# Kernel optimization log

Hardware: AMD Instinct MI355X
Metric: run time of the kernel (lower is better)

## Reference

```python
import jax, jax.numpy as jnp
import numpy as np

B, T, C = 8, 2048, 512
H = 16
HS = C // H  # 32, must equal HEAD_SIZE
TM_DIM = 32   # TIME_MIX_EXTRA_DIM
TD_DIM = 64   # TIME_DECAY_EXTRA_DIM
LAYER_ID, N_LAYER = 5, 12


def setup_inputs() -> dict:
    key = jax.random.key(0)
    ks = jax.random.split(key, 16)
    r01 = LAYER_ID / (N_LAYER - 1)
    r1a0 = 1.0 - LAYER_ID / N_LAYER
    ddd = (jnp.arange(C, dtype=jnp.float32) / C)
    n = jnp.arange(C, dtype=jnp.float32)
    decay_speed = -6.0 + 5.0 * (n / (C - 1)) ** (0.7 + 1.3 * r01)
    zigzag = ((n + 1) % 3 - 1) * 0.1
    faaaa = (r01 * (1 - n / (C - 1)) + zigzag).reshape(H, HS)
    s = 1.0 / np.sqrt(C)
    return {
        "x": jax.random.normal(ks[0], (B, T, C), dtype=jnp.float32),
        "time_maa_x": 1.0 - ddd ** r1a0,
        "time_maa_w": 1.0 - ddd ** r1a0,
        "time_maa_k": 1.0 - ddd ** r1a0,
        "time_maa_v": 1.0 - (ddd ** r1a0 + 0.3 * r01),
        "time_maa_r": 1.0 - ddd ** (0.5 * r1a0),
        "time_maa_g": 1.0 - ddd ** (0.5 * r1a0),
        "time_maa_w1": jax.random.uniform(ks[1], (C, TM_DIM * 5), minval=-1e-4, maxval=1e-4),
        "time_maa_w2": jax.random.uniform(ks[2], (5, TM_DIM, C), minval=-1e-4, maxval=1e-4),
        "time_decay": decay_speed,
        "time_decay_w1": jax.random.uniform(ks[3], (C, TD_DIM), minval=-1e-4, maxval=1e-4),
        "time_decay_w2": jax.random.uniform(ks[4], (TD_DIM, C), minval=-1e-4, maxval=1e-4),
        "time_faaaa": faaaa,
        "Wr": jax.random.normal(ks[5], (C, C)) * s,
        "Wk": jax.random.normal(ks[6], (C, C)) * s,
        "Wv": jax.random.normal(ks[7], (C, C)) * s,
        "Wg": jax.random.normal(ks[8], (C, C)) * s,
        "Wo": jax.random.normal(ks[9], (C, C)) * s,
        "ln_w": jnp.ones((C,), dtype=jnp.float32),
        "ln_b": jnp.zeros((C,), dtype=jnp.float32),
    }


def _wkv6(r, k, v, w, u):
    # r,k,v,w: (B,T,C); u: (H,HS). Linear recurrence per (batch, head).
    rs = r.reshape(B, T, H, HS).transpose(1, 0, 2, 3)
    ks_ = k.reshape(B, T, H, HS).transpose(1, 0, 2, 3)
    vs = v.reshape(B, T, H, HS).transpose(1, 0, 2, 3)
    # decay = exp(-exp(w)) per channel (the kernel passes ew = -exp(w))
    ds = jnp.exp(-jnp.exp(w.astype(jnp.float32))).reshape(B, T, H, HS).transpose(1, 0, 2, 3)
    ub = u[None, :, :, None]  # (1,H,HS_key,1)

    def step(S, inp):  # S: (B,H,HS_key,HS_val)
        r_t, k_t, v_t, d_t = inp
        kv = jnp.einsum("bhj,bhi->bhji", k_t, v_t)
        y = jnp.einsum("bhj,bhji->bhi", r_t, S + ub * kv)
        S = d_t[..., None] * S + kv
        return S, y

    S0 = jnp.zeros((B, H, HS, HS), dtype=jnp.float32)
    _, ys = jax.lax.scan(step, S0, (rs, ks_, vs, ds))
    return ys.transpose(1, 0, 2, 3).reshape(B, T, C)


def reference(x, time_maa_x, time_maa_w, time_maa_k, time_maa_v, time_maa_r,
              time_maa_g, time_maa_w1, time_maa_w2, time_decay, time_decay_w1,
              time_decay_w2, time_faaaa, Wr, Wk, Wv, Wg, Wo, ln_w, ln_b):
    # time shift: x_{t-1}, zeros at t=0  (ZeroPad2d((0,0,1,-1)))
    xshift = jnp.concatenate([jnp.zeros_like(x[:, :1]), x[:, :-1]], axis=1)
    xx = xshift - x
    xxx = x + xx * time_maa_x
    mix = jnp.tanh(jnp.einsum("btc,cd->btd", xxx, time_maa_w1)).reshape(B, T, 5, TM_DIM)
    mix = jnp.einsum("btfd,fdc->fbtc", mix, time_maa_w2)  # (5,B,T,C)
    mw, mk, mv, mr, mg = mix[0], mix[1], mix[2], mix[3], mix[4]
    xw = x + xx * (time_maa_w + mw)
    xk = x + xx * (time_maa_k + mk)
    xv = x + xx * (time_maa_v + mv)
    xr = x + xx * (time_maa_r + mr)
    xg = x + xx * (time_maa_g + mg)
    r = xr @ Wr.T
    k = xk @ Wk.T
    v = xv @ Wv.T
    g = jax.nn.silu(xg @ Wg.T)
    w = time_decay + jnp.tanh(xw @ time_decay_w1) @ time_decay_w2
    y = _wkv6(r, k, v, w, time_faaaa)
    # GroupNorm with H groups over channel dim, eps=1e-5
    yg = y.reshape(B, T, H, HS)
    mu = yg.mean(-1, keepdims=True)
    var = yg.var(-1, keepdims=True)
    yn = ((yg - mu) * jax.lax.rsqrt(var + 1e-5)).reshape(B, T, C)
    yn = yn * ln_w + ln_b
    return (yn * g) @ Wo.T
```

## Files before the change

kernel.cpp:

```cpp
#include <hip/hip_runtime.h>
#include <hip/hip_bf16.h>

#define B_ 8
#define T_ 2048
#define C_ 512
#define H_ 16
#define HS_ 32
#define BT_ (B_*T_)
#define CL_ 64
#define NC_ (T_/CL_)
#define STF_ 1056
#define WSZ_ 262144

typedef __hip_bfloat16 bf16;
typedef __attribute__((ext_vector_type(8))) short short8;
typedef __attribute__((ext_vector_type(4))) short short4v;
typedef __attribute__((ext_vector_type(4))) float f32x4;

__device__ __forceinline__ float b2f(bf16 v) { return __bfloat162float(v); }
__device__ __forceinline__ bf16 f2b(float v) { return __float2bfloat16(v); }
__device__ __forceinline__ float s2f(short s) {
  unsigned u = ((unsigned)(unsigned short)s) << 16;
  return __builtin_bit_cast(float, u);
}
__device__ __forceinline__ short f2s(float f) {
  bf16 b = f2b(f);
  return __builtin_bit_cast(short, b);
}

__device__ __forceinline__ void gl2lds(const void* g, void* l) {
  __builtin_amdgcn_global_load_lds(
      (const __attribute__((address_space(1))) void*)g,
      (__attribute__((address_space(3))) void*)l, 16, 0, 0);
}

__global__ __launch_bounds__(256) void prep_combo_kernel(
    const float* __restrict__ x, const float* __restrict__ tmx,
    const float* __restrict__ Wr, const float* __restrict__ Wk,
    const float* __restrict__ Wv, const float* __restrict__ Wg,
    const float* __restrict__ Wo, const float* __restrict__ w1,
    const float* __restrict__ wd1, const float* __restrict__ w2,
    bf16* __restrict__ xxx, bf16* __restrict__ Wrb, bf16* __restrict__ Wkb,
    bf16* __restrict__ Wvb, bf16* __restrict__ Wgb, bf16* __restrict__ Wob,
    bf16* __restrict__ w1p, bf16* __restrict__ wd1p, bf16* __restrict__ w2p) {
  int idx = blockIdx.x * 256 + threadIdx.x;
  if (idx < BT_ * C_) {
    int c = idx & (C_ - 1);
    int t = (idx >> 9) & (T_ - 1);
    float xc = x[idx];
    float xp = (t == 0) ? 0.f : x[idx - C_];
    xxx[idx] = f2b(xc + (xp - xc) * tmx[c]);
    return;
  }
  idx -= BT_ * C_;
  if (idx < 5 * WSZ_) {
    int w = idx >> 18;
    int i = idx & (WSZ_ - 1);
    const float* src = (w == 0) ? Wr : (w == 1) ? Wk : (w == 2) ? Wv
                     : (w == 3) ? Wg : Wo;
    bf16* dst = (w == 0) ? Wrb : (w == 1) ? Wkb : (w == 2) ? Wvb
              : (w == 3) ? Wgb : Wob;
    float s = src[i];
    bf16 hi = f2b(s);
    dst[i] = hi;
    dst[WSZ_ + i] = f2b(s - b2f(hi));
    return;
  }
  idx -= 5 * WSZ_;
  if (idx < 192 * 512) {
    int n = idx >> 9, k = idx & (C_ - 1);
    w1p[idx] = f2b(n < 160 ? w1[k * 160 + n] : 0.f);
    return;
  }
  idx -= 192 * 512;
  if (idx < 64 * 512) {
    int n = idx >> 9, k = idx & (C_ - 1);
    wd1p[idx] = f2b(wd1[k * 64 + n]);
    return;
  }
  idx -= 64 * 512;
  {
    int c = idx / 192, n = idx - c * 192;
    w2p[idx] = f2b(n < 160 ? w2[(size_t)n * C_ + c] : 0.f);
  }
}
#define PREP_N_ ((BT_*C_ + 5*WSZ_ + 192*512 + 64*512 + 512*192) / 256)

template<int BN, int MODE, int SPLIT>
__global__ __launch_bounds__(256) void mfma_gemm_kernel(
    const bf16* __restrict__ A, const bf16* __restrict__ Bw,
    void* __restrict__ O, int N) {
  constexpr int BM = 128, BK = 32;
  constexpr int AE = BM * BK / 8;
  constexpr int BE = BN * BK / 8;
  __shared__ short8 Asm[AE];
  __shared__ short8 Bsm[BE];
  __shared__ short8 Lsm[SPLIT ? BE : 1];
  const int tid = threadIdx.x;
  const int lane = tid & 63;
  const int wave = tid >> 6;
  const int m0 = blockIdx.x * BM;
  const int n0 = blockIdx.y * BN;
  const int wm = (BN == 128) ? (wave >> 1) * 64 : wave * 32;
  const int wn = (BN == 128) ? (wave & 1) * 64 : 0;
  constexpr int MT = (BN == 128) ? 4 : 2;
  constexpr int NT = 4;
  f32x4 acc[MT][NT] = {};
  const int e0 = tid, e1 = tid + 256;
  const int r0 = ((e0 >> 6) << 4) | (e0 & 15), q0 = (e0 >> 4) & 3;
  const int r1 = ((e1 >> 6) << 4) | (e1 & 15), q1 = (e1 >> 4) & 3;
  const unsigned short* Au = (const unsigned short*)A;
  const unsigned short* Bu = (const unsigned short*)Bw;
  const unsigned short* Lu = Bu + (SPLIT ? WSZ_ : 0);
  for (int k0 = 0; k0 < C_; k0 += BK) {
    __syncthreads();
    gl2lds(&Au[(size_t)(m0 + r0) * C_ + k0 + q0 * 8], &Asm[e0]);
    gl2lds(&Au[(size_t)(m0 + r1) * C_ + k0 + q1 * 8], &Asm[e1]);
    gl2lds(&Bu[(size_t)(n0 + r0) * C_ + k0 + q0 * 8], &Bsm[e0]);
    if constexpr (BN == 128)
      gl2lds(&Bu[(size_t)(n0 + r1) * C_ + k0 + q1 * 8], &Bsm[e1]);
    if constexpr (SPLIT) {
      gl2lds(&Lu[(size_t)(n0 + r0) * C_ + k0 + q0 * 8], &Lsm[e0]);
      if constexpr (BN == 128)
        gl2lds(&Lu[(size_t)(n0 + r1) * C_ + k0 + q1 * 8], &Lsm[e1]);
    }
    __syncthreads();
    short8 af[MT], bh[NT];
    #pragma unroll
    for (int mt = 0; mt < MT; ++mt) af[mt] = Asm[((wm >> 4) + mt) * 64 + lane];
    #pragma unroll
    for (int nt = 0; nt < NT; ++nt) bh[nt] = Bsm[((wn >> 4) + nt) * 64 + lane];
    #pragma unroll
    for (int mt = 0; mt < MT; ++mt)
      #pragma unroll
      for (int nt = 0; nt < NT; ++nt)
        acc[mt][nt] = __builtin_amdgcn_mfma_f32_16x16x32_bf16(
            af[mt], bh[nt], acc[mt][nt], 0, 0, 0);
    if constexpr (SPLIT) {
      short8 bl[NT];
      #pragma unroll
      for (int nt = 0; nt < NT; ++nt) bl[nt] = Lsm[((wn >> 4) + nt) * 64 + lane];
      #pragma unroll
      for (int mt = 0; mt < MT; ++mt)
        #pragma unroll
        for (int nt = 0; nt < NT; ++nt)
          acc[mt][nt] = __builtin_amdgcn_mfma_f32_16x16x32_bf16(
              af[mt], bl[nt], acc[mt][nt], 0, 0, 0);
    }
  }
  const int col = lane & 15, qr = lane >> 4;
  #pragma unroll
  for (int mt = 0; mt < MT; ++mt) {
    int mrow = m0 + wm + mt * 16 + qr * 4;
    #pragma unroll
    for (int nt = 0; nt < NT; ++nt) {
      int nc = n0 + wn + nt * 16 + col;
      #pragma unroll
      for (int r = 0; r < 4; ++r) {
        float v = acc[mt][nt][r];
        if (MODE == 1) v = v / (1.f + __expf(-v));
        if (MODE == 3) v = tanhf(v);
        size_t oi = (size_t)(mrow + r) * N + nc;
        if (MODE == 2) ((float*)O)[oi] = v;
        else           ((bf16*)O)[oi] = f2b(v);
      }
    }
  }
}

__global__ __launch_bounds__(256) void proj4_gemm_kernel(
    const bf16* __restrict__ A0, const bf16* __restrict__ B0, bf16* __restrict__ O0,
    const bf16* __restrict__ A1, const bf16* __restrict__ B1, bf16* __restrict__ O1,
    const bf16* __restrict__ A2, const bf16* __restrict__ B2, bf16* __restrict__ O2,
    const bf16* __restrict__ A3, const bf16* __restrict__ B3, bf16* __restrict__ O3) {
  constexpr int BM = 128, BN = 128, BK = 32;
  __shared__ short8 Asm[BM * BK / 8];
  __shared__ short8 Bsm[BN * BK / 8];
  __shared__ short8 Lsm[BN * BK / 8];
  const int zz = blockIdx.z;
  const bf16* A  = (zz == 0) ? A0 : (zz == 1) ? A1 : (zz == 2) ? A2 : A3;
  const bf16* Bw = (zz == 0) ? B0 : (zz == 1) ? B1 : (zz == 2) ? B2 : B3;
  bf16* O        = (zz == 0) ? O0 : (zz == 1) ? O1 : (zz == 2) ? O2 : O3;
  const bool silu = (zz == 3);
  const int tid = threadIdx.x;
  const int lane = tid & 63;
  const int wave = tid >> 6;
  const int m0 = blockIdx.x * BM;
  const int n0 = blockIdx.y * BN;
  const int wm = (wave >> 1) * 64;
  const int wn = (wave & 1) * 64;
  constexpr int MT = 4, NT = 4;
  f32x4 acc[MT][NT] = {};
  const int e0 = tid, e1 = tid + 256;
  const int r0 = ((e0 >> 6) << 4) | (e0 & 15), q0 = (e0 >> 4) & 3;
  const int r1 = ((e1 >> 6) << 4) | (e1 & 15), q1 = (e1 >> 4) & 3;
  const unsigned short* Au = (const unsigned short*)A;
  const unsigned short* Bu = (const unsigned short*)Bw;
  const unsigned short* Lu = Bu + WSZ_;
  for (int k0 = 0; k0 < C_; k0 += BK) {
    __syncthreads();
    gl2lds(&Au[(size_t)(m0 + r0) * C_ + k0 + q0 * 8], &Asm[e0]);
    gl2lds(&Au[(size_t)(m0 + r1) * C_ + k0 + q1 * 8], &Asm[e1]);
    gl2lds(&Bu[(size_t)(n0 + r0) * C_ + k0 + q0 * 8], &Bsm[e0]);
    gl2lds(&Bu[(size_t)(n0 + r1) * C_ + k0 + q1 * 8], &Bsm[e1]);
    gl2lds(&Lu[(size_t)(n0 + r0) * C_ + k0 + q0 * 8], &Lsm[e0]);
    gl2lds(&Lu[(size_t)(n0 + r1) * C_ + k0 + q1 * 8], &Lsm[e1]);
    __syncthreads();
    short8 af[MT], bh[NT];
    #pragma unroll
    for (int mt = 0; mt < MT; ++mt) af[mt] = Asm[((wm >> 4) + mt) * 64 + lane];
    #pragma unroll
    for (int nt = 0; nt < NT; ++nt) bh[nt] = Bsm[((wn >> 4) + nt) * 64 + lane];
    #pragma unroll
    for (int mt = 0; mt < MT; ++mt)
      #pragma unroll
      for (int nt = 0; nt < NT; ++nt)
        acc[mt][nt] = __builtin_amdgcn_mfma_f32_16x16x32_bf16(
            af[mt], bh[nt], acc[mt][nt], 0, 0, 0);
    short8 bl[NT];
    #pragma unroll
    for (int nt = 0; nt < NT; ++nt) bl[nt] = Lsm[((wn >> 4) + nt) * 64 + lane];
    #pragma unroll
    for (int mt = 0; mt < MT; ++mt)
      #pragma unroll
      for (int nt = 0; nt < NT; ++nt)
        acc[mt][nt] = __builtin_amdgcn_mfma_f32_16x16x32_bf16(
            af[mt], bl[nt], acc[mt][nt], 0, 0, 0);
  }
  const int col = lane & 15, qr = lane >> 4;
  #pragma unroll
  for (int mt = 0; mt < MT; ++mt) {
    int mrow = m0 + wm + mt * 16 + qr * 4;
    #pragma unroll
    for (int nt = 0; nt < NT; ++nt) {
      int nc = n0 + wn + nt * 16 + col;
      #pragma unroll
      for (int r = 0; r < 4; ++r) {
        float v = acc[mt][nt][r];
        if (silu) v = v / (1.f + __expf(-v));
        O[(size_t)(mrow + r) * C_ + nc] = f2b(v);
      }
    }
  }
}

__global__ __launch_bounds__(256) void mix_mfma_kernel(
    const bf16* __restrict__ mix5, const bf16* __restrict__ w2p,
    const float* __restrict__ x,
    const float* __restrict__ tmw, const float* __restrict__ tmk,
    const float* __restrict__ tmv, const float* __restrict__ tmr,
    const float* __restrict__ tmg,
    bf16* __restrict__ xw, bf16* __restrict__ xk, bf16* __restrict__ xv,
    bf16* __restrict__ xr, bf16* __restrict__ xg) {
  constexpr int LDP = 200;
  __shared__ __align__(16) unsigned short Asm[64 * LDP];
  __shared__ __align__(16) unsigned short Bsm[64 * LDP];
  const int tid = threadIdx.x;
  const int row0 = blockIdx.x * 64;
  const int col0 = blockIdx.y * 64;
  const unsigned short* Au = (const unsigned short*)mix5;
  const unsigned short* Bu = (const unsigned short*)w2p;
  #pragma unroll
  for (int e0 = 0; e0 < 64 * 20; e0 += 256) {
    int e = e0 + tid;
    int rr = e / 20, p = e - rr * 20;
    *(short8*)&Asm[rr * LDP + p * 8] =
        *(const short8*)&Au[(size_t)(row0 + rr) * 192 + p * 8];
    *(short8*)&Bsm[rr * LDP + p * 8] =
        *(const short8*)&Bu[(size_t)(col0 + rr) * 192 + p * 8];
  }
  __syncthreads();
  const int lane = tid & 63, wave = tid >> 6;
  const int fl = lane & 15, q = lane >> 4;
  short8 af[5];
  #pragma unroll
  for (int f = 0; f < 5; ++f)
    af[f] = *(const short8*)&Asm[(wave * 16 + fl) * LDP + f * 32 + q * 8];
  f32x4 acc[4][5] = {};
  #pragma unroll
  for (int nt = 0; nt < 4; ++nt)
    #pragma unroll
    for (int f = 0; f < 5; ++f) {
      short8 bfr = *(const short8*)&Bsm[(nt * 16 + fl) * LDP + f * 32 + q * 8];
      acc[nt][f] = __builtin_amdgcn_mfma_f32_16x16x32_bf16(
          af[f], bfr, acc[nt][f], 0, 0, 0);
    }
  #pragma unroll
  for (int nt = 0; nt < 4; ++nt) {
    int cc = col0 + nt * 16 + fl;
    float vw = tmw[cc], vk = tmk[cc], vv = tmv[cc], vr = tmr[cc],
          vg = tmg[cc];
    #pragma unroll
    for (int r = 0; r < 4; ++r) {
      int rr = row0 + wave * 16 + q * 4 + r;
      size_t idx = (size_t)rr * C_ + cc;
      float xc = x[idx];
      float xx = (((rr & (T_ - 1)) == 0) ? 0.f : x[idx - C_]) - xc;
      xw[idx] = f2b(xc + xx * (vw + acc[nt][0][r]));
      xk[idx] = f2b(xc + xx * (vk + acc[nt][1][r]));
      xv[idx] = f2b(xc + xx * (vv + acc[nt][2][r]));
      xr[idx] = f2b(xc + xx * (vr + acc[nt][3][r]));
      xg[idx] = f2b(xc + xx * (vg + acc[nt][4][r]));
    }
  }
}

__global__ __launch_bounds__(512) void decay_kernel(
    const bf16* __restrict__ h1, const float* __restrict__ wd2,
    const float* __restrict__ tdecay, bf16* __restrict__ ee) {
  __shared__ float Hs[8][64];
  int row0 = blockIdx.x * 8;
  {
    int e = threadIdx.x;
    Hs[e >> 6][e & 63] = b2f(h1[(size_t)(row0 + (e >> 6)) * 64 + (e & 63)]);
  }
  __syncthreads();
  int c = threadIdx.x;
  float acc[8] = {0.f,0.f,0.f,0.f,0.f,0.f,0.f,0.f};
  for (int j = 0; j < 64; ++j) {
    float wv = wd2[j * C_ + c];
    #pragma unroll
    for (int r = 0; r < 8; ++r) acc[r] += Hs[r][j] * wv;
  }
  float td = tdecay[c];
  #pragma unroll
  for (int r = 0; r < 8; ++r)
    ee[(size_t)(row0 + r) * C_ + c] = f2b(expf(td + acc[r]));
}

__global__ __launch_bounds__(256) void wkv_partial_mfma(
    const bf16* __restrict__ k, const bf16* __restrict__ v,
    const bf16* __restrict__ ee, float* __restrict__ st) {
  __shared__ __align__(16) char smem[17536];
  float* Lm  = (float*)smem;
  bf16*  K2T = (bf16*)(smem + 8320);
  bf16*  VT  = (bf16*)(smem + 12928);
  bf16*  Eb  = K2T;
  int g = blockIdx.x;
  int bh = g >> 5, c = g & (NC_ - 1);
  int b = bh >> 4, h = bh & 15;
  const int tid = threadIdx.x;
  const int lane = tid & 63, wave = tid >> 6;
  const int tl = lane >> 3;
  const int c4 = (lane & 7) * 4;
  size_t gbase = (size_t)b * T_ * C_ + (size_t)(c * CL_) * C_ + h * HS_;
  const short* ku = (const short*)k;
  const short* vu = (const short*)v;
  const short* eu = (const short*)ee;
  #pragma unroll
  for (int it = 0; it < 2; ++it) {
    int e4 = it * 256 + tid;
    int row = e4 >> 3, cc = (e4 & 7) * 4;
    short4v ev = *(const short4v*)&eu[gbase + (size_t)row * C_ + cc];
    *(short4v*)&((short*)Eb)[row * 32 + cc] = ev;
  }
  short4v k4[2], v4[2];
  #pragma unroll
  for (int it2 = 0; it2 < 2; ++it2) {
    int t = wave * 16 + it2 * 8 + tl;
    k4[it2] = *(const short4v*)&ku[gbase + (size_t)t * C_ + c4];
    v4[it2] = *(const short4v*)&vu[gbase + (size_t)t * C_ + c4];
  }
  __syncthreads();
  if (tid < 32) {
    float L = 0.f;
    for (int t = 0; t < CL_; ++t) {
      Lm[t * 32 + tid] = L;
      L -= b2f(Eb[t * 32 + tid]);
    }
    Lm[64 * 32 + tid] = L;
  }
  __syncthreads();
  f32x4 Ltot4 = *(const f32x4*)&Lm[64 * 32 + c4];
  #pragma unroll
  for (int it2 = 0; it2 < 2; ++it2) {
    int t = wave * 16 + it2 * 8 + tl;
    f32x4 Lt14 = *(const f32x4*)&Lm[(t + 1) * 32 + c4];
    #pragma unroll
    for (int j = 0; j < 4; ++j) {
      ((short*)K2T)[(c4 + j) * 72 + t] =
          f2s(s2f(k4[it2][j]) * __expf(Ltot4[j] - Lt14[j]));
      ((short*)VT)[(c4 + j) * 72 + t] = v4[it2][j];
    }
  }
  __syncthreads();
  const int fl = lane & 15, q = lane >> 4;
  const int mt = wave >> 1, nt = wave & 1;
  f32x4 accS = {};
  #pragma unroll
  for (int kc = 0; kc < 2; ++kc) {
    short8 av = *(const short8*)(VT + (mt * 16 + fl) * 72 + kc * 32 + q * 8);
    short8 bk = *(const short8*)(K2T + (nt * 16 + fl) * 72 + kc * 32 + q * 8);
    accS = __builtin_amdgcn_mfma_f32_16x16x32_bf16(av, bk, accS, 0, 0, 0);
  }
  size_t sbase = (size_t)g * STF_;
  #pragma unroll
  for (int r = 0; r < 4; ++r)
    st[sbase + (size_t)(mt * 16 + q * 4 + r) * 32 + nt * 16 + fl] = accS[r];
  if (tid < 32) st[sbase + 1024 + tid] = __expf(Lm[64 * 32 + tid]);
}

__global__ __launch_bounds__(64) void wkv_stitch_kernel(float* __restrict__ st) {
  int bh = blockIdx.x;
  int lane = threadIdx.x;
  int i = lane & 31, half = lane >> 5;
  float R[16];
  #pragma unroll
  for (int jj = 0; jj < 16; ++jj) R[jj] = 0.f;
  size_t s0 = (size_t)bh * NC_ * STF_;
  const int off = i * 32 + (half << 4);
  const int poff = 1024 + (half << 4);
  f32x4 Sc[4], Pj[4];
  {
    const f32x4* sp = (const f32x4*)(st + s0 + off);
    const f32x4* pp = (const f32x4*)(st + s0 + poff);
    #pragma unroll
    for (int q = 0; q < 4; ++q) { Sc[q] = sp[q]; Pj[q] = pp[q]; }
  }
  for (int c = 0; c < NC_; ++c) {
    size_t s = s0 + (size_t)c * STF_;
    f32x4 Sn[4], Pn[4];
    if (c + 1 < NC_) {
      const f32x4* sp = (const f32x4*)(st + s + STF_ + off);
      const f32x4* pp = (const f32x4*)(st + s + STF_ + poff);
      #pragma unroll
      for (int q = 0; q < 4; ++q) { Sn[q] = sp[q]; Pn[q] = pp[q]; }
    }
    if (c > 0) {
      __align__(16) short hi16[16], lo16[16];
      #pragma unroll
      for (int jj = 0; jj < 16; ++jj) {
        short hb = f2s(R[jj]);
        hi16[jj] = hb;
        lo16[jj] = f2s(R[jj] - s2f(hb));
      }
      short* sb = (short*)(st + s - STF_);
      *(short8*)&sb[off]         = *(const short8*)&hi16[0];
      *(short8*)&sb[off + 8]     = *(const short8*)&hi16[8];
      *(short8*)&sb[1024 + off]     = *(const short8*)&lo16[0];
      *(short8*)&sb[1024 + off + 8] = *(const short8*)&lo16[8];
    }
    #pragma unroll
    for (int q = 0; q < 4; ++q)
      #pragma unroll
      for (int j = 0; j < 4; ++j)
        R[q * 4 + j] = fmaf(Pj[q][j], R[q * 4 + j], Sc[q][j]);
    if (c + 1 < NC_) {
      #pragma unroll
      for (int q = 0; q < 4; ++q) { Sc[q] = Sn[q]; Pj[q] = Pn[q]; }
    }
  }
}

__global__ __launch_bounds__(256) void wkv_final_mfma(
    const bf16* __restrict__ r, const bf16* __restrict__ k,
    const bf16* __restrict__ v, const bf16* __restrict__ ee,
    const float* __restrict__ faaaa, const float* __restrict__ st,
    const bf16* __restrict__ gg, const float* __restrict__ lnw,
    const float* __restrict__ lnb, bf16* __restrict__ z) {
  __shared__ __align__(16) char smem[24320];
  float* Lm = (float*)smem;
  bf16*  Pm = (bf16*)smem;
  bf16*  RA = (bf16*)(smem + 9216);
  bf16*  Kd = (bf16*)(smem + 14336);
  bf16*  VT = (bf16*)(smem + 19456);
  bf16*  Eb = VT;
  float* bon = (float*)(smem + 24064);
  int g = blockIdx.x;
  int bh = g >> 5, c = g & (NC_ - 1);
  int b = bh >> 4, h = bh & 15;
  const int tid = threadIdx.x;
  const int lane = tid & 63, wave = tid >> 6;
  const int tl = lane >> 3;
  const int c4 = (lane & 7) * 4;
  const int fl = lane & 15, q = lane >> 4;
  size_t gbase = (size_t)b * T_ * C_ + (size_t)(c * CL_) * C_ + h * HS_;
  size_t sbase = (size_t)g * STF_;
  const short* ru = (const short*)r;
  const short* ku = (const short*)k;
  const short* vu = (const short*)v;
  const short* eu = (const short*)ee;
  #pragma unroll
  for (int it = 0; it < 2; ++it) {
    int e4 = it * 256 + tid;
    int row = e4 >> 3, cc = (e4 & 7) * 4;
    short4v ev = *(const short4v*)&eu[gbase + (size_t)row * C_ + cc];
    *(short4v*)&((short*)Eb)[row * 32 + cc] = ev;
  }
  short8 sh[2] = {}, sl[2] = {};
  if (c != 0) {
    const unsigned short* sb = (const unsigned short*)(st + sbase - STF_);
    #pragma unroll
    for (int nt = 0; nt < 2; ++nt) {
      sh[nt] = *(const short8*)&sb[(nt * 16 + fl) * 32 + q * 8];
      sl[nt] = *(const short8*)&sb[1024 + (nt * 16 + fl) * 32 + q * 8];
    }
  }
  short4v r4[2], k4[2], v4[2];
  #pragma unroll
  for (int it2 = 0; it2 < 2; ++it2) {
    int t = wave * 16 + it2 * 8 + tl;
    size_t gi = gbase + (size_t)t * C_ + c4;
    r4[it2] = *(const short4v*)&ru[gi];
    k4[it2] = *(const short4v*)&ku[gi];
    v4[it2] = *(const short4v*)&vu[gi];
  }
  __syncthreads();
  if (tid < 32) {
    float L = 0.f;
    for (int t = 0; t < CL_; ++t) {
      Lm[t * 32 + tid] = L;
      L -= b2f(Eb[t * 32 + tid]);
    }
    Lm[64 * 32 + tid] = L;
  }
  __syncthreads();
  f32x4 u4 = *(const f32x4*)&faaaa[h * HS_ + c4];
  #pragma unroll
  for (int it2 = 0; it2 < 2; ++it2) {
    int t = wave * 16 + it2 * 8 + tl;
    f32x4 Lt4  = *(const f32x4*)&Lm[t * 32 + c4];
    f32x4 Lt14 = *(const f32x4*)&Lm[(t + 1) * 32 + c4];
    short4v ra4, kd4;
    float pb = 0.f;
    #pragma unroll
    for (int j = 0; j < 4; ++j) {
      float rvj = s2f(r4[it2][j]);
      float kvj = s2f(k4[it2][j]);
      ra4[j] = f2s(rvj * __expf(Lt4[j]));
      kd4[j] = f2s(kvj * __expf(-Lt14[j]));
      ((short*)VT)[(c4 + j) * 72 + t] = v4[it2][j];
      pb += rvj * u4[j] * kvj;
    }
    *(short4v*)&((short*)RA)[t * 40 + c4] = ra4;
    *(short4v*)&((short*)Kd)[t * 40 + c4] = kd4;
    pb += __shfl_xor(pb, 1); pb += __shfl_xor(pb, 2); pb += __shfl_xor(pb, 4);
    if ((lane & 7) == 0) bon[t] = pb;
  }
  __syncthreads();
  short8 afr = *(const short8*)(RA + (wave * 16 + fl) * 40 + q * 8);
  f32x4 accY[2] = {};
  #pragma unroll
  for (int nt = 0; nt < 2; ++nt) {
    accY[nt] = __builtin_amdgcn_mfma_f32_16x16x32_bf16(afr, sh[nt], accY[nt], 0, 0, 0);
    accY[nt] = __builtin_amdgcn_mfma_f32_16x16x32_bf16(afr, sl[nt], accY[nt], 0, 0, 0);
  }
  f32x4 accP[4] = {};
  #pragma unroll
  for (int s4 = 0; s4 < 4; ++s4) {
    short8 bk = *(const short8*)(Kd + (s4 * 16 + fl) * 40 + q * 8);
    accP[s4] = __builtin_amdgcn_mfma_f32_16x16x32_bf16(afr, bk, accP[s4], 0, 0, 0);
  }
  #pragma unroll
  for (int s4 = 0; s4 < 4; ++s4)
    #pragma unroll
    for (int rr = 0; rr < 4; ++rr) {
      int t = wave * 16 + q * 4 + rr;
      int s = s4 * 16 + fl;
      float pv = accP[s4][rr];
      float bv = bon[t];
      pv = (s < t) ? pv : ((s == t) ? bv : 0.f);
      Pm[t * 72 + s] = f2b(pv);
    }
  __syncthreads();
  #pragma unroll
  for (int kc = 0; kc < 2; ++kc) {
    short8 ap = *(const short8*)(Pm + (wave * 16 + fl) * 72 + kc * 32 + q * 8);
    #pragma unroll
    for (int nt = 0; nt < 2; ++nt) {
      short8 bv = *(const short8*)(VT + (nt * 16 + fl) * 72 + kc * 32 + q * 8);
      accY[nt] = __builtin_amdgcn_mfma_f32_16x16x32_bf16(ap, bv, accY[nt], 0, 0, 0);
    }
  }
  float lw0 = lnw[h * HS_ + fl],      lb0 = lnb[h * HS_ + fl];
  float lw1 = lnw[h * HS_ + 16 + fl], lb1 = lnb[h * HS_ + 16 + fl];
  #pragma unroll
  for (int rr = 0; rr < 4; ++rr) {
    int t = wave * 16 + q * 4 + rr;
    float a0 = accY[0][rr], a1 = accY[1][rr];
    float mu = a0 + a1;
    mu += __shfl_xor(mu, 1); mu += __shfl_xor(mu, 2);
    mu += __shfl_xor(mu, 4); mu += __shfl_xor(mu, 8);
    mu *= (1.f / 32.f);
    float d0 = a0 - mu, d1 = a1 - mu;
    float ss = d0 * d0 + d1 * d1;
    ss += __shfl_xor(ss, 1); ss += __shfl_xor(ss, 2);
    ss += __shfl_xor(ss, 4); ss += __shfl_xor(ss, 8);
    float rs = rsqrtf(ss * (1.f / 32.f) + 1e-5f);
    size_t gi = gbase + (size_t)t * C_;
    float g0 = b2f(gg[gi + fl]);
    float g1 = b2f(gg[gi + 16 + fl]);
    z[gi + fl]      = f2b((d0 * rs * lw0 + lb0) * g0);
    z[gi + 16 + fl] = f2b((d1 * rs * lw1 + lb1) * g1);
  }
}

extern "C" void kernel_launch(void* const* d_in, const int* in_sizes, int n_in,
                              void* d_out, int out_size, void* d_ws, size_t ws_size,
                              hipStream_t stream) {
  (void)in_sizes; (void)n_in; (void)out_size; (void)ws_size;
  const float* x      = (const float*)d_in[0];
  const float* tmx    = (const float*)d_in[1];
  const float* tmw    = (const float*)d_in[2];
  const float* tmk    = (const float*)d_in[3];
  const float* tmv    = (const float*)d_in[4];
  const float* tmr    = (const float*)d_in[5];
  const float* tmg    = (const float*)d_in[6];
  const float* w1     = (const float*)d_in[7];
  const float* w2     = (const float*)d_in[8];
  const float* tdecay = (const float*)d_in[9];
  const float* wd1    = (const float*)d_in[10];
  const float* wd2    = (const float*)d_in[11];
  const float* faaaa  = (const float*)d_in[12];
  const float* Wr     = (const float*)d_in[13];
  const float* Wk     = (const float*)d_in[14];
  const float* Wv     = (const float*)d_in[15];
  const float* Wg     = (const float*)d_in[16];
  const float* Wo     = (const float*)d_in[17];
  const float* lnw    = (const float*)d_in[18];
  const float* lnb    = (const float*)d_in[19];
  float* out = (float*)d_out;

  char* w8 = (char*)d_ws;
  const size_t MB = 1024ull * 1024ull;
  bf16* S0 = (bf16*)(w8 +  0 * MB);
  bf16* S1 = (bf16*)(w8 + 16 * MB);
  bf16* S2 = (bf16*)(w8 + 32 * MB);
  bf16* S3 = (bf16*)(w8 + 48 * MB);
  bf16* S4 = (bf16*)(w8 + 64 * MB);
  bf16* S5 = (bf16*)(w8 + 80 * MB);
  float* st = (float*)(w8 + 96 * MB);
  char* wreg = w8 + 112 * MB + 512 * 1024;
  bf16* S6 = (bf16*)(w8 + 120 * MB);
  bf16* S7 = (bf16*)(w8 + 136 * MB);
  bf16* S8 = (bf16*)(w8 + 152 * MB);
  bf16* Wrb  = (bf16*)(wreg);
  bf16* Wkb  = Wrb + 2 * WSZ_;
  bf16* Wvb  = Wkb + 2 * WSZ_;
  bf16* Wgb  = Wvb + 2 * WSZ_;
  bf16* Wob  = Wgb + 2 * WSZ_;
  bf16* w1p  = Wob + 2 * WSZ_;
  bf16* wd1p = w1p + 192 * 512;
  bf16* w2p  = wd1p + 64 * 512;
  bf16* mix5p = S5;
  bf16* h1    = S5 + (size_t)BT_ * 192;

  prep_combo_kernel<<<PREP_N_, 256, 0, stream>>>(
      x, tmx, Wr, Wk, Wv, Wg, Wo, w1, wd1, w2,
      S0, Wrb, Wkb, Wvb, Wgb, Wob, w1p, wd1p, w2p);
  mfma_gemm_kernel<64, 3, 0><<<dim3(128, 3), 256, 0, stream>>>(S0, w1p, mix5p, 192);
  mix_mfma_kernel<<<dim3(BT_ / 64, 8), 256, 0, stream>>>(
      mix5p, w2p, x, tmw, tmk, tmv, tmr, tmg, S0, S1, S2, S3, S4);
  mfma_gemm_kernel<64, 3, 0><<<dim3(128, 1), 256, 0, stream>>>(S0, wd1p, h1, 64);
  decay_kernel<<<BT_ / 8, 512, 0, stream>>>(h1, wd2, tdecay, S0);
  proj4_gemm_kernel<<<dim3(128, 4, 4), 256, 0, stream>>>(
      S3, Wrb, S6,  S1, Wkb, S7,  S2, Wvb, S8,  S4, Wgb, S5);
  wkv_partial_mfma<<<B_ * H_ * NC_, 256, 0, stream>>>(S7, S8, S0, st);
  wkv_stitch_kernel<<<B_ * H_, 64, 0, stream>>>(st);
  wkv_final_mfma<<<B_ * H_ * NC_, 256, 0, stream>>>(S6, S7, S8, S0, faaaa, st,
                                                    S5, lnw, lnb, S1);
  mfma_gemm_kernel<128, 2, 1><<<dim3(128, 4), 256, 0, stream>>>(S1, Wob, out, C_);
}
```

Measured before the change: 419.5 us.

## Double-buffer LDS tiles in MFMA GEMM kernels to overlap loads with compute

Both MFMA GEMM kernels now keep two LDS buffers per operand. The next K-slice is issued with direct global-to-LDS loads before computing on the current slice, and a partial vmcnt wait plus raw s_barrier calls replace the paired __syncthreads. This aims to hide global load latency behind the MFMA work. In exchange LDS use doubles, which may lower occupancy, and correctness now depends on the hand-written vmcnt counts matching the number of loads issued per stage.

```diff
diff --git a/kernel.cpp b/kernel.cpp
--- a/kernel.cpp
+++ b/kernel.cpp
@@ -93,9 +93,11 @@
   constexpr int BM = 128, BK = 32;
   constexpr int AE = BM * BK / 8;
   constexpr int BE = BN * BK / 8;
-  __shared__ short8 Asm[AE];
-  __shared__ short8 Bsm[BE];
-  __shared__ short8 Lsm[SPLIT ? BE : 1];
+  constexpr int NL = 2 + (BN == 128 ? 2 : 1) * (1 + SPLIT);
+  constexpr int NK = C_ / BK;
+  __shared__ short8 Asm[2 * AE];
+  __shared__ short8 Bsm[2 * BE];
+  __shared__ short8 Lsm[SPLIT ? 2 * BE : 2];
   const int tid = threadIdx.x;
   const int lane = tid & 63;
   const int wave = tid >> 6;
@@ -112,24 +114,35 @@
   const unsigned short* Au = (const unsigned short*)A;
   const unsigned short* Bu = (const unsigned short*)Bw;
   const unsigned short* Lu = Bu + (SPLIT ? WSZ_ : 0);
-  for (int k0 = 0; k0 < C_; k0 += BK) {
-    __syncthreads();
-    gl2lds(&Au[(size_t)(m0 + r0) * C_ + k0 + q0 * 8], &Asm[e0]);
-    gl2lds(&Au[(size_t)(m0 + r1) * C_ + k0 + q1 * 8], &Asm[e1]);
-    gl2lds(&Bu[(size_t)(n0 + r0) * C_ + k0 + q0 * 8], &Bsm[e0]);
+  auto stage = [&](int buf, int k0) {
+    gl2lds(&Au[(size_t)(m0 + r0) * C_ + k0 + q0 * 8], &Asm[buf * AE + e0]);
+    gl2lds(&Au[(size_t)(m0 + r1) * C_ + k0 + q1 * 8], &Asm[buf * AE + e1]);
+    gl2lds(&Bu[(size_t)(n0 + r0) * C_ + k0 + q0 * 8], &Bsm[buf * BE + e0]);
     if constexpr (BN == 128)
-      gl2lds(&Bu[(size_t)(n0 + r1) * C_ + k0 + q1 * 8], &Bsm[e1]);
+      gl2lds(&Bu[(size_t)(n0 + r1) * C_ + k0 + q1 * 8], &Bsm[buf * BE + e1]);
     if constexpr (SPLIT) {
-      gl2lds(&Lu[(size_t)(n0 + r0) * C_ + k0 + q0 * 8], &Lsm[e0]);
+      gl2lds(&Lu[(size_t)(n0 + r0) * C_ + k0 + q0 * 8], &Lsm[buf * BE + e0]);
       if constexpr (BN == 128)
-        gl2lds(&Lu[(size_t)(n0 + r1) * C_ + k0 + q1 * 8], &Lsm[e1]);
-    }
-    __syncthreads();
+        gl2lds(&Lu[(size_t)(n0 + r1) * C_ + k0 + q1 * 8], &Lsm[buf * BE + e1]);
+    }
+  };
+  stage(0, 0);
+  for (int i = 0; i < NK; ++i) {
+    if (i + 1 < NK) {
+      stage((i + 1) & 1, (i + 1) * BK);
+      asm volatile("s_waitcnt vmcnt(%0)" :: "i"(NL) : "memory");
+    } else {
+      asm volatile("s_waitcnt vmcnt(0)" ::: "memory");
+    }
+    __builtin_amdgcn_s_barrier();
+    __builtin_amdgcn_sched_barrier(0);
+    const short8* Ab = Asm + (i & 1) * AE;
+    const short8* Bb = Bsm + (i & 1) * BE;
     short8 af[MT], bh[NT];
     #pragma unroll
-    for (int mt = 0; mt < MT; ++mt) af[mt] = Asm[((wm >> 4) + mt) * 64 + lane];
-    #pragma unroll
-    for (int nt = 0; nt < NT; ++nt) bh[nt] = Bsm[((wn >> 4) + nt) * 64 + lane];
+    for (int mt = 0; mt < MT; ++mt) af[mt] = Ab[((wm >> 4) + mt) * 64 + lane];
+    #pragma unroll
+    for (int nt = 0; nt < NT; ++nt) bh[nt] = Bb[((wn >> 4) + nt) * 64 + lane];
     #pragma unroll
     for (int mt = 0; mt < MT; ++mt)
       #pragma unroll
@@ -137,9 +150,10 @@
         acc[mt][nt] = __builtin_amdgcn_mfma_f32_16x16x32_bf16(
             af[mt], bh[nt], acc[mt][nt], 0, 0, 0);
     if constexpr (SPLIT) {
+      const short8* Lb = Lsm + (i & 1) * BE;
       short8 bl[NT];
       #pragma unroll
-      for (int nt = 0; nt < NT; ++nt) bl[nt] = Lsm[((wn >> 4) + nt) * 64 + lane];
+      for (int nt = 0; nt < NT; ++nt) bl[nt] = Lb[((wn >> 4) + nt) * 64 + lane];
       #pragma unroll
       for (int mt = 0; mt < MT; ++mt)
         #pragma unroll
@@ -147,6 +161,8 @@
           acc[mt][nt] = __builtin_amdgcn_mfma_f32_16x16x32_bf16(
               af[mt], bl[nt], acc[mt][nt], 0, 0, 0);
     }
+    __builtin_amdgcn_sched_barrier(0);
+    __builtin_amdgcn_s_barrier();
   }
   const int col = lane & 15, qr = lane >> 4;
   #pragma unroll
@@ -174,9 +190,11 @@
     const bf16* __restrict__ A2, const bf16* __restrict__ B2, bf16* __restrict__ O2,
     const bf16* __restrict__ A3, const bf16* __restrict__ B3, bf16* __restrict__ O3) {
   constexpr int BM = 128, BN = 128, BK = 32;
-  __shared__ short8 Asm[BM * BK / 8];
-  __shared__ short8 Bsm[BN * BK / 8];
-  __shared__ short8 Lsm[BN * BK / 8];
+  constexpr int AE = BM * BK / 8, BE = BN * BK / 8;
+  constexpr int NL = 6, NK = C_ / BK;
+  __shared__ short8 Asm[2 * AE];
+  __shared__ short8 Bsm[2 * BE];
+  __shared__ short8 Lsm[2 * BE];
   const int zz = blockIdx.z;
   const bf16* A  = (zz == 0) ? A0 : (zz == 1) ? A1 : (zz == 2) ? A2 : A3;
   const bf16* Bw = (zz == 0) ? B0 : (zz == 1) ? B1 : (zz == 2) ? B2 : B3;
@@ -197,20 +215,32 @@
   const unsigned short* Au = (const unsigned short*)A;
   const unsigned short* Bu = (const unsigned short*)Bw;
   const unsigned short* Lu = Bu + WSZ_;
-  for (int k0 = 0; k0 < C_; k0 += BK) {
-    __syncthreads();
-    gl2lds(&Au[(size_t)(m0 + r0) * C_ + k0 + q0 * 8], &Asm[e0]);
-    gl2lds(&Au[(size_t)(m0 + r1) * C_ + k0 + q1 * 8], &Asm[e1]);
-    gl2lds(&Bu[(size_t)(n0 + r0) * C_ + k0 + q0 * 8], &Bsm[e0]);
-    gl2lds(&Bu[(size_t)(n0 + r1) * C_ + k0 + q1 * 8], &Bsm[e1]);
-    gl2lds(&Lu[(size_t)(n0 + r0) * C_ + k0 + q0 * 8], &Lsm[e0]);
-    gl2lds(&Lu[(size_t)(n0 + r1) * C_ + k0 + q1 * 8], &Lsm[e1]);
-    __syncthreads();
+  auto stage = [&](int buf, int k0) {
+    gl2lds(&Au[(size_t)(m0 + r0) * C_ + k0 + q0 * 8], &Asm[buf * AE + e0]);
+    gl2lds(&Au[(size_t)(m0 + r1) * C_ + k0 + q1 * 8], &Asm[buf * AE + e1]);
+    gl2lds(&Bu[(size_t)(n0 + r0) * C_ + k0 + q0 * 8], &Bsm[buf * BE + e0]);
+    gl2lds(&Bu[(size_t)(n0 + r1) * C_ + k0 + q1 * 8], &Bsm[buf * BE + e1]);
+    gl2lds(&Lu[(size_t)(n0 + r0) * C_ + k0 + q0 * 8], &Lsm[buf * BE + e0]);
+    gl2lds(&Lu[(size_t)(n0 + r1) * C_ + k0 + q1 * 8], &Lsm[buf * BE + e1]);
+  };
+  stage(0, 0);
+  for (int i = 0; i < NK; ++i) {
+    if (i + 1 < NK) {
+      stage((i + 1) & 1, (i + 1) * BK);
+      asm volatile("s_waitcnt vmcnt(%0)" :: "i"(NL) : "memory");
+    } else {
+      asm volatile("s_waitcnt vmcnt(0)" ::: "memory");
+    }
+    __builtin_amdgcn_s_barrier();
+    __builtin_amdgcn_sched_barrier(0);
+    const short8* Ab = Asm + (i & 1) * AE;
+    const short8* Bb = Bsm + (i & 1) * BE;
+    const short8* Lb = Lsm + (i & 1) * BE;
     short8 af[MT], bh[NT];
     #pragma unroll
-    for (int mt = 0; mt < MT; ++mt) af[mt] = Asm[((wm >> 4) + mt) * 64 + lane];
-    #pragma unroll
-    for (int nt = 0; nt < NT; ++nt) bh[nt] = Bsm[((wn >> 4) + nt) * 64 + lane];
+    for (int mt = 0; mt < MT; ++mt) af[mt] = Ab[((wm >> 4) + mt) * 64 + lane];
+    #pragma unroll
+    for (int nt = 0; nt < NT; ++nt) bh[nt] = Bb[((wn >> 4) + nt) * 64 + lane];
     #pragma unroll
     for (int mt = 0; mt < MT; ++mt)
       #pragma unroll
@@ -219,13 +249,15 @@
             af[mt], bh[nt], acc[mt][nt], 0, 0, 0);
     short8 bl[NT];
     #pragma unroll
-    for (int nt = 0; nt < NT; ++nt) bl[nt] = Lsm[((wn >> 4) + nt) * 64 + lane];
+    for (int nt = 0; nt < NT; ++nt) bl[nt] = Lb[((wn >> 4) + nt) * 64 + lane];
     #pragma unroll
     for (int mt = 0; mt < MT; ++mt)
       #pragma unroll
       for (int nt = 0; nt < NT; ++nt)
         acc[mt][nt] = __builtin_amdgcn_mfma_f32_16x16x32_bf16(
             af[mt], bl[nt], acc[mt][nt], 0, 0, 0);
+    __builtin_amdgcn_sched_barrier(0);
+    __builtin_amdgcn_s_barrier();
   }
   const int col = lane & 15, qr = lane >> 4;
   #pragma unroll
```

Measured after the change: 421.7 us. Within noise of the previous version (+0.5%).
